# Kernel tuning notes

Hardware: AMD Instinct MI355X
Metric: run time of the kernel (lower is better)

The kernel has to match this reference:

```python
import jax, jax.numpy as jnp
import numpy as np

N_BLOCKS = 64
BLOCK_R = 128  # rows per block (output features per block)
BLOCK_C = 128  # cols per block (input features per block)
BATCH = 4096

def setup_inputs() -> dict:
    key = jax.random.key(0)
    k1, k2 = jax.random.split(key)
    x = jax.random.normal(k1, (BATCH, N_BLOCKS * BLOCK_C), dtype=jnp.float32)
    # learned parameters: diagonal blocks, torch.randn init
    blocks = jax.random.normal(k2, (N_BLOCKS, BLOCK_R, BLOCK_C), dtype=jnp.float32)
    return {"x": x, "blocks": blocks}

def reference(x, blocks):
    # Equivalent to x @ full_matrix.T where full_matrix = blockdiag(blocks),
    # but computed directly on the blocks (no zero-fill materialization).
    B = x.shape[0]
    n, r, c = blocks.shape
    xb = x.reshape(B, n, c)                      # split input into per-block column slices
    out = jnp.einsum('bnc,nrc->bnr', xb, blocks)  # per-block GEMM: x_slice @ block.T
    return out.reshape(B, n * r)
```

## Files before the change

kernel.cpp:

```cpp
#include <hip/hip_runtime.h>
#include <hip/hip_bf16.h>


typedef __bf16 bf16_8 __attribute__((ext_vector_type(8)));
typedef __bf16 bf16_4 __attribute__((ext_vector_type(4)));
typedef float f32x4 __attribute__((ext_vector_type(4)));

#define LDS_K 136

__global__ __launch_bounds__(256, 3)
void BlocDiagLinear_kernel(const float* __restrict__ x,
                           const float* __restrict__ blocks,
                           float* __restrict__ out)
{
    __shared__ __align__(16) __bf16 ws[128 * LDS_K];

    const int bid = blockIdx.x;
    const int nb  = bid & 63;
    const int mt  = bid >> 6;

    const int t  = threadIdx.x;
    const int c4 = t & 31;
    const int r0 = t >> 5;

    const float* wg = blocks + (size_t)nb * 16384;
#pragma unroll
    for (int i = 0; i < 16; ++i) {
        const int row = i * 8 + r0;
        const float4 vw = *(const float4*)(wg + row * 128 + c4 * 4);
        bf16_4 bw = { (__bf16)vw.x, (__bf16)vw.y, (__bf16)vw.z, (__bf16)vw.w };
        *(bf16_4*)(ws + row * LDS_K + c4 * 4) = bw;
    }
    __syncthreads();

    const int lane = t & 63;
    const int w    = t >> 6;
    const int wm   = w >> 1;
    const int wn   = w & 1;
    const int lm   = lane & 15;
    const int q    = lane >> 4;

    const float* xb = x + (size_t)(mt * 128 + wn * 64 + lm) * 8192
                        + (size_t)nb * 128 + q * 8;

    f32x4 acc[4][4];
#pragma unroll
    for (int mi = 0; mi < 4; ++mi)
#pragma unroll
        for (int ni = 0; ni < 4; ++ni)
            acc[mi][ni] = (f32x4){0.f, 0.f, 0.f, 0.f};

    float4 raw[8];
#pragma unroll
    for (int kk = 0; kk < 4; ++kk) {
        raw[2 * kk]     = *(const float4*)(xb + kk * 32);
        raw[2 * kk + 1] = *(const float4*)(xb + kk * 32 + 4);
    }

#pragma unroll
    for (int ni = 0; ni < 4; ++ni) {
        bf16_8 b[4];
#pragma unroll
        for (int kk = 0; kk < 4; ++kk) {
            const float4 lo = raw[2 * kk];
            const float4 hi = raw[2 * kk + 1];
            b[kk] = (bf16_8){ (__bf16)lo.x, (__bf16)lo.y, (__bf16)lo.z, (__bf16)lo.w,
                              (__bf16)hi.x, (__bf16)hi.y, (__bf16)hi.z, (__bf16)hi.w };
        }
        if (ni < 3) {
            const float* p = xb + (size_t)(ni + 1) * 16 * 8192;
#pragma unroll
            for (int kk = 0; kk < 4; ++kk) {
                raw[2 * kk]     = *(const float4*)(p + kk * 32);
                raw[2 * kk + 1] = *(const float4*)(p + kk * 32 + 4);
            }
        }
#pragma unroll
        for (int kk = 0; kk < 4; ++kk) {
            bf16_8 a[4];
#pragma unroll
            for (int mi = 0; mi < 4; ++mi)
                a[mi] = *(const bf16_8*)(ws + (wm * 64 + mi * 16 + lm) * LDS_K
                                            + kk * 32 + q * 8);
#pragma unroll
            for (int mi = 0; mi < 4; ++mi)
                acc[mi][ni] = __builtin_amdgcn_mfma_f32_16x16x32_bf16(
                                  a[mi], b[kk], acc[mi][ni], 0, 0, 0);
        }
    }

    float* og = out + (size_t)(mt * 128 + wn * 64 + lm) * 8192
                    + (size_t)nb * 128 + wm * 64 + q * 4;
#pragma unroll
    for (int ni = 0; ni < 4; ++ni)
#pragma unroll
        for (int mi = 0; mi < 4; ++mi)
            *(f32x4*)(og + (size_t)ni * 16 * 8192 + mi * 16) = acc[mi][ni];
}

extern "C" void kernel_launch(void* const* d_in, const int* in_sizes, int n_in,
                              void* d_out, int out_size, void* d_ws, size_t ws_size,
                              hipStream_t stream) {
    const float* x      = (const float*)d_in[0];
    const float* blocks = (const float*)d_in[1];
    float* out          = (float*)d_out;
    BlocDiagLinear_kernel<<<dim3(64 * 32), dim3(256), 0, stream>>>(x, blocks, out);
}
```

Baseline: 246.8 us.

## Repartition warps over batch rows, swizzle LDS, and prefetch x before weight staging

Measured after the change: 307.2 us. 1.25x slower.

```diff
diff --git a/kernel.cpp b/kernel.cpp
--- a/kernel.cpp
+++ b/kernel.cpp
@@ -6,95 +6,88 @@
 typedef __bf16 bf16_4 __attribute__((ext_vector_type(4)));
 typedef float f32x4 __attribute__((ext_vector_type(4)));
 
-#define LDS_K 136
-
-__global__ __launch_bounds__(256, 3)
+__global__ __launch_bounds__(256, 5)
 void BlocDiagLinear_kernel(const float* __restrict__ x,
                            const float* __restrict__ blocks,
                            float* __restrict__ out)
 {
-    __shared__ __align__(16) __bf16 ws[128 * LDS_K];
+    __shared__ __align__(16) __bf16 ws[128 * 128];
 
     const int bid = blockIdx.x;
     const int nb  = bid & 63;
     const int mt  = bid >> 6;
 
-    const int t  = threadIdx.x;
+    const int t    = threadIdx.x;
+    const int lane = t & 63;
+    const int w    = t >> 6;
+    const int lm   = lane & 15;
+    const int q    = lane >> 4;
+
+    const float* xb = x + (size_t)(mt * 128 + w * 32 + lm) * 8192
+                        + (size_t)nb * 128 + q * 8;
+    float4 raw[16];
+#pragma unroll
+    for (int ni = 0; ni < 2; ++ni)
+#pragma unroll
+        for (int kk = 0; kk < 4; ++kk) {
+            const float* p = xb + (size_t)ni * 16 * 8192 + kk * 32;
+            raw[ni * 8 + 2 * kk]     = *(const float4*)(p);
+            raw[ni * 8 + 2 * kk + 1] = *(const float4*)(p + 4);
+        }
+
     const int c4 = t & 31;
     const int r0 = t >> 5;
-
     const float* wg = blocks + (size_t)nb * 16384;
+    char* wsb = (char*)ws;
 #pragma unroll
     for (int i = 0; i < 16; ++i) {
         const int row = i * 8 + r0;
         const float4 vw = *(const float4*)(wg + row * 128 + c4 * 4);
         bf16_4 bw = { (__bf16)vw.x, (__bf16)vw.y, (__bf16)vw.z, (__bf16)vw.w };
-        *(bf16_4*)(ws + row * LDS_K + c4 * 4) = bw;
+        *(bf16_4*)(wsb + ((row * 256 + c4 * 8) ^ (r0 << 4))) = bw;
     }
     __syncthreads();
 
-    const int lane = t & 63;
-    const int w    = t >> 6;
-    const int wm   = w >> 1;
-    const int wn   = w & 1;
-    const int lm   = lane & 15;
-    const int q    = lane >> 4;
-
-    const float* xb = x + (size_t)(mt * 128 + wn * 64 + lm) * 8192
-                        + (size_t)nb * 128 + q * 8;
-
-    f32x4 acc[4][4];
+    f32x4 acc[8][2];
 #pragma unroll
-    for (int mi = 0; mi < 4; ++mi)
+    for (int mi = 0; mi < 8; ++mi)
 #pragma unroll
-        for (int ni = 0; ni < 4; ++ni)
+        for (int ni = 0; ni < 2; ++ni)
             acc[mi][ni] = (f32x4){0.f, 0.f, 0.f, 0.f};
 
-    float4 raw[8];
-#pragma unroll
-    for (int kk = 0; kk < 4; ++kk) {
-        raw[2 * kk]     = *(const float4*)(xb + kk * 32);
-        raw[2 * kk + 1] = *(const float4*)(xb + kk * 32 + 4);
-    }
+    const int swz = (lm & 7) << 4;
 
 #pragma unroll
-    for (int ni = 0; ni < 4; ++ni) {
+    for (int ni = 0; ni < 2; ++ni) {
         bf16_8 b[4];
 #pragma unroll
         for (int kk = 0; kk < 4; ++kk) {
-            const float4 lo = raw[2 * kk];
-            const float4 hi = raw[2 * kk + 1];
+            const float4 lo = raw[ni * 8 + 2 * kk];
+            const float4 hi = raw[ni * 8 + 2 * kk + 1];
             b[kk] = (bf16_8){ (__bf16)lo.x, (__bf16)lo.y, (__bf16)lo.z, (__bf16)lo.w,
                               (__bf16)hi.x, (__bf16)hi.y, (__bf16)hi.z, (__bf16)hi.w };
         }
-        if (ni < 3) {
-            const float* p = xb + (size_t)(ni + 1) * 16 * 8192;
-#pragma unroll
-            for (int kk = 0; kk < 4; ++kk) {
-                raw[2 * kk]     = *(const float4*)(p + kk * 32);
-                raw[2 * kk + 1] = *(const float4*)(p + kk * 32 + 4);
-            }
-        }
 #pragma unroll
         for (int kk = 0; kk < 4; ++kk) {
-            bf16_8 a[4];
+            bf16_8 a[8];
 #pragma unroll
-            for (int mi = 0; mi < 4; ++mi)
-                a[mi] = *(const bf16_8*)(ws + (wm * 64 + mi * 16 + lm) * LDS_K
-                                            + kk * 32 + q * 8);
+            for (int mi = 0; mi < 8; ++mi) {
+                const int byte = ((mi * 16 + lm) * 256 + kk * 64 + q * 16) ^ swz;
+                a[mi] = *(const bf16_8*)(wsb + byte);
+            }
 #pragma unroll
-            for (int mi = 0; mi < 4; ++mi)
+            for (int mi = 0; mi < 8; ++mi)
                 acc[mi][ni] = __builtin_amdgcn_mfma_f32_16x16x32_bf16(
                                   a[mi], b[kk], acc[mi][ni], 0, 0, 0);
         }
     }
 
-    float* og = out + (size_t)(mt * 128 + wn * 64 + lm) * 8192
-                    + (size_t)nb * 128 + wm * 64 + q * 4;
+    float* og = out + (size_t)(mt * 128 + w * 32 + lm) * 8192
+                    + (size_t)nb * 128 + q * 4;
 #pragma unroll
-    for (int ni = 0; ni < 4; ++ni)
+    for (int ni = 0; ni < 2; ++ni)
 #pragma unroll
-        for (int mi = 0; mi < 4; ++mi)
+        for (int mi = 0; mi < 8; ++mi)
             *(f32x4*)(og + (size_t)ni * 16 * 8192 + mi * 16) = acc[mi][ni];
 }
 
```
